# Kernel tuning notes

Measured on AMD Instinct MI355X. Metric: run time of the kernel, lower is better.

Reference implementation:

```python
import jax, jax.numpy as jnp
import numpy as np

N = 50000
E = 600000
IN_DIM = 128
D = 32          # out_dim per head
H = 4           # heads
M = 3           # num metapaths
HID = 128       # semantic attention hidden
NEG_SLOPE = 0.2


def setup_inputs() -> dict:
    key = jax.random.key(0)
    ks = jax.random.split(key, 12)
    x = jax.random.normal(ks[0], (N, IN_DIM), dtype=jnp.float32)
    mp_edge_index = jax.random.randint(ks[1], (M, 2, E), 0, N, dtype=jnp.int64)
    s = 1.0 / np.sqrt(IN_DIM)
    W = jax.random.normal(ks[2], (M, IN_DIM, H * D), dtype=jnp.float32) * s
    att_src = jax.random.normal(ks[3], (M, H, D), dtype=jnp.float32) * (1.0 / np.sqrt(D))
    att_dst = jax.random.normal(ks[4], (M, H, D), dtype=jnp.float32) * (1.0 / np.sqrt(D))
    bias = jnp.zeros((M, H * D), dtype=jnp.float32)
    ln_gamma = jnp.ones((H * D,), dtype=jnp.float32)
    ln_beta = jnp.zeros((H * D,), dtype=jnp.float32)
    sem_W1 = jax.random.normal(ks[5], (H * D, HID), dtype=jnp.float32) * (1.0 / np.sqrt(H * D))
    sem_b1 = jnp.zeros((HID,), dtype=jnp.float32)
    sem_W2 = jax.random.normal(ks[6], (HID, 1), dtype=jnp.float32) * (1.0 / np.sqrt(HID))
    return dict(x=x, mp_edge_index=mp_edge_index, W=W, att_src=att_src,
                att_dst=att_dst, bias=bias, ln_gamma=ln_gamma, ln_beta=ln_beta,
                sem_W1=sem_W1, sem_b1=sem_b1, sem_W2=sem_W2)


def _gat_conv(x, edge_index, W_m, a_src, a_dst, b_m):
    # PyG GATConv (add_self_loops=True, concat=True). x: [N, F_in]
    n = x.shape[0]
    h = (x @ W_m).reshape(n, H, D)                       # [N, H, D]
    loops = jnp.arange(n, dtype=edge_index.dtype)
    src = jnp.concatenate([edge_index[0], loops])        # [E+N]
    dst = jnp.concatenate([edge_index[1], loops])
    alpha_s = jnp.einsum('nhd,hd->nh', h, a_src)         # [N, H]
    alpha_d = jnp.einsum('nhd,hd->nh', h, a_dst)
    e = jax.nn.leaky_relu(alpha_s[src] + alpha_d[dst], NEG_SLOPE)  # [E+N, H]
    # segment softmax over edges grouped by destination node
    e_max = jax.ops.segment_max(e, dst, num_segments=n)
    e = jnp.exp(e - e_max[dst])
    denom = jax.ops.segment_sum(e, dst, num_segments=n)
    alpha = e / (denom[dst] + 1e-16)                     # [E+N, H]
    msg = h[src] * alpha[:, :, None]                     # [E+N, H, D]
    out = jax.ops.segment_sum(msg, dst, num_segments=n)  # [N, H, D]
    return out.reshape(n, H * D) + b_m


def _layer_norm(y, gamma, beta):
    mu = y.mean(-1, keepdims=True)
    var = y.var(-1, keepdims=True)
    return (y - mu) * jax.lax.rsqrt(var + 1e-5) * gamma + beta


def reference(x, mp_edge_index, W, att_src, att_dst, bias, ln_gamma, ln_beta,
              sem_W1, sem_b1, sem_W2):
    embs = []
    for i in range(M):
        emb = _gat_conv(x, mp_edge_index[i], W[i], att_src[i], att_dst[i], bias[i])
        emb = jax.nn.elu(_layer_norm(emb, ln_gamma, ln_beta))
        embs.append(emb)
    z = jnp.stack(embs, axis=1)                          # [N, M, H*D]
    # semantic attention
    w = (jnp.tanh(z @ sem_W1 + sem_b1) @ sem_W2).mean(0)  # [M, 1]
    beta = jax.nn.softmax(w, axis=0)                      # [M, 1]
    out_emb = (beta[None, :, :] * z).sum(1)               # [N, H*D]
    att_mp = beta.squeeze()                               # [M]
    return out_emb, att_mp
```

## Files before the change

### kernel.cpp

```cpp
#include <hip/hip_runtime.h>
#include <hip/hip_bf16.h>

#define N_NODES 50000
#define N_EDGES 600000
#define NMETA   3
#define NEG_SLOPE 0.2f
#define LTOT (NMETA * N_NODES)
#define SPAN_SHIFT 9
#define NBUCK 98
#define BCAP 8192

typedef unsigned short u16;
typedef short bf16x8 __attribute__((ext_vector_type(8)));
typedef float f32x4 __attribute__((ext_vector_type(4)));

__device__ __forceinline__ float bf2f(u16 v) {
    union { unsigned int u; float f; } x; x.u = ((unsigned int)v) << 16; return x.f;
}
__device__ __forceinline__ u16 f2bf(float f) {
    return __hip_bfloat16_raw(__float2bfloat16(f)).x;
}

__global__ __launch_bounds__(256) void k_prep_x(
    const float* __restrict__ x, u16* __restrict__ xb)
{
    int i = blockIdx.x * 256 + threadIdx.x;
    if (i >= N_NODES * 32) return;
    float4 v = ((const float4*)x)[i];
    ushort4 o;
    o.x = f2bf(v.x); o.y = f2bf(v.y); o.z = f2bf(v.z); o.w = f2bf(v.w);
    ((ushort4*)xb)[i] = o;
}

__global__ __launch_bounds__(256) void k_prep_w(
    const float* __restrict__ W, const float* __restrict__ W1,
    u16* __restrict__ WT, u16* __restrict__ W1T)
{
    int idx = blockIdx.x * 256 + threadIdx.x;
    if (idx < NMETA * 16384) {
        int m = idx >> 14, r = idx & 16383;
        int col = r >> 7, k = r & 127;
        WT[idx] = f2bf(W[(m << 14) + k * 128 + col]);
    } else {
        int r = idx - NMETA * 16384;
        int col = r >> 7, k = r & 127;
        W1T[r] = f2bf(W1[k * 128 + col]);
    }
}

__global__ __launch_bounds__(256) void k_gemm_h(
    const u16* __restrict__ xb,
    const u16* __restrict__ WT,
    const float* __restrict__ att_src,
    const float* __restrict__ att_dst,
    u16* __restrict__ h,
    float* __restrict__ alpha_s,
    float* __restrict__ alpha_d)
{
    const int m = blockIdx.y;
    const int wv = threadIdx.x >> 6, lane = threadIdx.x & 63;
    const int row0 = (blockIdx.x * 4 + wv) * 16;
    if (row0 >= N_NODES) return;
    const int lhi = lane >> 4, llo = lane & 15;
    const u16* xrow = xb + (size_t)(row0 + llo) * 128 + lhi * 8;
    bf16x8 a[4];
    #pragma unroll
    for (int ks = 0; ks < 4; ++ks) a[ks] = *(const bf16x8*)(xrow + ks * 32);
    const u16* wbase = WT + (size_t)m * 16384 + (size_t)llo * 128 + lhi * 8;
    u16* hm = h + ((size_t)m * N_NODES + row0) * 128;
    float sp[4][4], dp[4][4];
    #pragma unroll
    for (int i = 0; i < 4; ++i)
        #pragma unroll
        for (int r = 0; r < 4; ++r) { sp[i][r] = 0.f; dp[i][r] = 0.f; }
    #pragma unroll
    for (int cf = 0; cf < 8; ++cf) {
        f32x4 acc = {0.f, 0.f, 0.f, 0.f};
        const u16* wp = wbase + cf * 16 * 128;
        #pragma unroll
        for (int ks = 0; ks < 4; ++ks) {
            bf16x8 b = *(const bf16x8*)(wp + ks * 32);
            acc = __builtin_amdgcn_mfma_f32_16x16x32_bf16(a[ks], b, acc, 0, 0, 0);
        }
        const int col = cf * 16 + llo;
        const int hh = cf >> 1;
        const float as = att_src[m * 128 + col];
        const float ad = att_dst[m * 128 + col];
        #pragma unroll
        for (int r = 0; r < 4; ++r) {
            hm[(size_t)(lhi * 4 + r) * 128 + col] = f2bf(acc[r]);
            sp[hh][r] += acc[r] * as;
            dp[hh][r] += acc[r] * ad;
        }
    }
    #pragma unroll
    for (int o = 1; o <= 8; o <<= 1) {
        #pragma unroll
        for (int i = 0; i < 4; ++i)
            #pragma unroll
            for (int r = 0; r < 4; ++r) {
                sp[i][r] += __shfl_xor(sp[i][r], o);
                dp[i][r] += __shfl_xor(dp[i][r], o);
            }
    }
    if (llo == 0) {
        #pragma unroll
        for (int r = 0; r < 4; ++r) {
            int n = row0 + lhi * 4 + r;
            f32x4 vs = {sp[0][r], sp[1][r], sp[2][r], sp[3][r]};
            f32x4 vd = {dp[0][r], dp[1][r], dp[2][r], dp[3][r]};
            *(f32x4*)(alpha_s + ((size_t)m * N_NODES + n) * 4) = vs;
            *(f32x4*)(alpha_d + ((size_t)m * N_NODES + n) * 4) = vd;
        }
    }
}

__global__ __launch_bounds__(256) void k_csrA(
    const int* __restrict__ ei, int* __restrict__ gcnt,
    unsigned long long* __restrict__ pairs)
{
    const int m = blockIdx.y;
    __shared__ int cnt[NBUCK];
    __shared__ int gbase[NBUCK];
    const int t = threadIdx.x;
    if (t < NBUCK) cnt[t] = 0;
    __syncthreads();
    const int e0 = blockIdx.x * 4096;
    const int* srcp = ei + (size_t)m * 2 * N_EDGES;
    const int* dstp = srcp + N_EDGES;
    int sa[16], da[16], sl[16];
    #pragma unroll
    for (int j = 0; j < 16; ++j) {
        int e = e0 + j * 256 + t;
        if (e < N_EDGES) {
            int s = srcp[e], d = dstp[e];
            if ((unsigned)s >= N_NODES) s = 0;
            if ((unsigned)d >= N_NODES) d = 0;
            sa[j] = s; da[j] = d;
            sl[j] = atomicAdd(&cnt[d >> SPAN_SHIFT], 1);
        } else sl[j] = -1;
    }
    __syncthreads();
    if (t < NBUCK) gbase[t] = atomicAdd(&gcnt[m * NBUCK + t], cnt[t]);
    __syncthreads();
    #pragma unroll
    for (int j = 0; j < 16; ++j) {
        if (sl[j] < 0) continue;
        int b = da[j] >> SPAN_SHIFT;
        int pos = gbase[b] + sl[j];
        if (pos < BCAP)
            pairs[(size_t)(m * NBUCK + b) * BCAP + pos] =
                ((unsigned long long)(da[j] & 511) << 32) | (unsigned)(sa[j] * 128);
    }
}

__global__ __launch_bounds__(256) void k_csrB(
    const int* __restrict__ gcnt, const unsigned long long* __restrict__ pairs,
    int* __restrict__ row_start, int* __restrict__ row_end, int* __restrict__ eidx)
{
    const int m = blockIdx.y, b = blockIdx.x;
    const int t = threadIdx.x;
    __shared__ int cnt[512];
    __shared__ int off[512];
    __shared__ int wsum[4];
    int nb = gcnt[m * NBUCK + b]; if (nb > BCAP) nb = BCAP;
    const int base = (m * NBUCK + b) * BCAP;
    cnt[t] = 0; cnt[t + 256] = 0;
    __syncthreads();
    for (int e = t; e < nb; e += 256) {
        int dl = (int)(pairs[(size_t)base + e] >> 32);
        atomicAdd(&cnt[dl], 1);
    }
    __syncthreads();
    int v0 = cnt[2 * t], v1 = cnt[2 * t + 1];
    int s = v0 + v1;
    int lane = t & 63, wv = t >> 6;
    int incl = s;
    #pragma unroll
    for (int o = 1; o < 64; o <<= 1) {
        int u = __shfl_up(incl, o);
        if (lane >= o) incl += u;
    }
    if (lane == 63) wsum[wv] = incl;
    __syncthreads();
    int woff = 0;
    for (int i = 0; i < wv; ++i) woff += wsum[i];
    int ex = woff + incl - s;
    off[2 * t] = ex;
    off[2 * t + 1] = ex + v0;
    __syncthreads();
    const int node0 = b << SPAN_SHIFT;
    for (int i = t; i < 512; i += 256) {
        int n = node0 + i;
        if (n < N_NODES) {
            int st = base + off[i];
            row_start[m * N_NODES + n] = st;
            row_end[m * N_NODES + n]   = st + cnt[i];
        }
    }
    __syncthreads();
    for (int e = t; e < nb; e += 256) {
        unsigned long long p = pairs[(size_t)base + e];
        int dl = (int)(p >> 32);
        int pos = atomicAdd(&off[dl], 1);
        eidx[(size_t)base + pos] = (int)(unsigned)p;
    }
}

__global__ __launch_bounds__(256) void k_gather(
    const int* __restrict__ row_start, const int* __restrict__ row_end,
    const int* __restrict__ eidx,
    const float* __restrict__ alpha_s, const float* __restrict__ alpha_d,
    const u16* __restrict__ h,
    const float* __restrict__ bias, const float* __restrict__ gamma,
    const float* __restrict__ lbeta,
    u16* __restrict__ z)
{
    long long w = ((long long)blockIdx.x * blockDim.x + threadIdx.x) >> 6;
    if (w >= (long long)LTOT) return;
    int m = (int)(w / N_NODES), n = (int)(w % N_NODES);
    int lane = threadIdx.x & 63, hh = lane >> 4;
    const float* as_m = alpha_s + (size_t)m * N_NODES * 4;
    const float* ad_m = alpha_d + (size_t)m * N_NODES * 4;
    const u16*   h_m  = h + (size_t)m * N_NODES * 128;
    float ad = ad_m[n * 4 + hh];
    float pre = as_m[n * 4 + hh] + ad;
    pre = pre > 0.f ? pre : NEG_SLOPE * pre;
    float ev = __expf(pre);
    float esum = ev;
    ushort2 hv = *(const ushort2*)(h_m + n * 128 + lane * 2);
    float acc0 = ev * bf2f(hv.x), acc1 = ev * bf2f(hv.y);
    int p = row_start[m * N_NODES + n];
    const int end = row_end[m * N_NODES + n];
    for (; p + 3 < end; p += 4) {
        int o1 = eidx[p], o2 = eidx[p + 1], o3 = eidx[p + 2], o4 = eidx[p + 3];
        float p1 = as_m[(o1 >> 5) + hh] + ad;
        float p2 = as_m[(o2 >> 5) + hh] + ad;
        float p3 = as_m[(o3 >> 5) + hh] + ad;
        float p4 = as_m[(o4 >> 5) + hh] + ad;
        ushort2 h1 = *(const ushort2*)(h_m + o1 + lane * 2);
        ushort2 h2 = *(const ushort2*)(h_m + o2 + lane * 2);
        ushort2 h3 = *(const ushort2*)(h_m + o3 + lane * 2);
        ushort2 h4 = *(const ushort2*)(h_m + o4 + lane * 2);
        p1 = p1 > 0.f ? p1 : NEG_SLOPE * p1;
        p2 = p2 > 0.f ? p2 : NEG_SLOPE * p2;
        p3 = p3 > 0.f ? p3 : NEG_SLOPE * p3;
        p4 = p4 > 0.f ? p4 : NEG_SLOPE * p4;
        float e1 = __expf(p1), e2 = __expf(p2), e3 = __expf(p3), e4 = __expf(p4);
        esum += (e1 + e2) + (e3 + e4);
        acc0 += e1 * bf2f(h1.x) + e2 * bf2f(h2.x) + e3 * bf2f(h3.x) + e4 * bf2f(h4.x);
        acc1 += e1 * bf2f(h1.y) + e2 * bf2f(h2.y) + e3 * bf2f(h3.y) + e4 * bf2f(h4.y);
    }
    for (; p < end; ++p) {
        int o1 = eidx[p];
        float p1 = as_m[(o1 >> 5) + hh] + ad;
        ushort2 h1 = *(const ushort2*)(h_m + o1 + lane * 2);
        p1 = p1 > 0.f ? p1 : NEG_SLOPE * p1;
        float e1 = __expf(p1);
        esum += e1;
        acc0 += e1 * bf2f(h1.x);
        acc1 += e1 * bf2f(h1.y);
    }
    float rinv = 1.f / (esum + 1e-16f);
    float v0 = acc0 * rinv + bias[m * 128 + lane * 2];
    float v1 = acc1 * rinv + bias[m * 128 + lane * 2 + 1];
    float s1 = v0 + v1, s2 = v0 * v0 + v1 * v1;
    #pragma unroll
    for (int o = 32; o >= 1; o >>= 1) { s1 += __shfl_xor(s1, o); s2 += __shfl_xor(s2, o); }
    float mu = s1 * (1.f / 128.f);
    float var = s2 * (1.f / 128.f) - mu * mu;
    float rs = rsqrtf(var + 1e-5f);
    float o0 = (v0 - mu) * rs * gamma[lane * 2]     + lbeta[lane * 2];
    float o1 = (v1 - mu) * rs * gamma[lane * 2 + 1] + lbeta[lane * 2 + 1];
    o0 = o0 > 0.f ? o0 : (__expf(o0) - 1.f);
    o1 = o1 > 0.f ? o1 : (__expf(o1) - 1.f);
    ushort2 outv; outv.x = f2bf(o0); outv.y = f2bf(o1);
    *(ushort2*)(z + ((size_t)n * NMETA + m) * 128 + lane * 2) = outv;
}

__global__ __launch_bounds__(256) void k_sem(
    const u16* __restrict__ z,
    const u16* __restrict__ W1T,
    const float* __restrict__ b1,
    const float* __restrict__ W2,
    float* __restrict__ wpart)
{
    __shared__ float part[NMETA];
    const int t = threadIdx.x;
    if (t < NMETA) part[t] = 0.f;
    __syncthreads();
    const int wv = t >> 6, lane = t & 63;
    const int row0 = (blockIdx.x * 4 + wv) * 16;
    if (row0 < LTOT) {
        const int lhi = lane >> 4, llo = lane & 15;
        const u16* zrow = z + (size_t)(row0 + llo) * 128 + lhi * 8;
        bf16x8 a[4];
        #pragma unroll
        for (int ks = 0; ks < 4; ++ks) a[ks] = *(const bf16x8*)(zrow + ks * 32);
        const u16* wb = W1T + (size_t)llo * 128 + lhi * 8;
        float rowacc[4] = {0.f, 0.f, 0.f, 0.f};
        #pragma unroll
        for (int cf = 0; cf < 8; ++cf) {
            f32x4 acc = {0.f, 0.f, 0.f, 0.f};
            const u16* wp = wb + cf * 16 * 128;
            #pragma unroll
            for (int ks = 0; ks < 4; ++ks) {
                bf16x8 bb = *(const bf16x8*)(wp + ks * 32);
                acc = __builtin_amdgcn_mfma_f32_16x16x32_bf16(a[ks], bb, acc, 0, 0, 0);
            }
            int col = cf * 16 + llo;
            float b1v = b1[col], w2v = W2[col];
            #pragma unroll
            for (int r = 0; r < 4; ++r)
                rowacc[r] += tanhf(acc[r] + b1v) * w2v;
        }
        #pragma unroll
        for (int o = 1; o <= 8; o <<= 1) {
            #pragma unroll
            for (int r = 0; r < 4; ++r) rowacc[r] += __shfl_xor(rowacc[r], o);
        }
        if (llo == 0) {
            #pragma unroll
            for (int r = 0; r < 4; ++r)
                atomicAdd(&part[(row0 + lhi * 4 + r) % NMETA], rowacc[r]);
        }
    }
    __syncthreads();
    if (t < NMETA) atomicAdd(&wpart[t], part[t]);
}

__global__ void k_beta(const float* __restrict__ wpart, float* __restrict__ betab,
                       float* __restrict__ attout)
{
    if (threadIdx.x == 0 && blockIdx.x == 0) {
        float w0 = wpart[0] * (1.f / N_NODES);
        float w1 = wpart[1] * (1.f / N_NODES);
        float w2 = wpart[2] * (1.f / N_NODES);
        float mx = fmaxf(w0, fmaxf(w1, w2));
        float e0 = __expf(w0 - mx), e1 = __expf(w1 - mx), e2 = __expf(w2 - mx);
        float s = 1.f / (e0 + e1 + e2);
        float b0 = e0 * s, b1 = e1 * s, b2 = e2 * s;
        betab[0] = b0; betab[1] = b1; betab[2] = b2;
        attout[0] = b0; attout[1] = b1; attout[2] = b2;
    }
}

__global__ __launch_bounds__(256) void k_combine(
    const u16* __restrict__ z, const float* __restrict__ betab,
    float* __restrict__ out)
{
    int idx = blockIdx.x * blockDim.x + threadIdx.x;
    if (idx >= N_NODES * 64) return;
    int n = idx >> 6, c2 = (idx & 63) * 2;
    float b0 = betab[0], b1 = betab[1], b2 = betab[2];
    const u16* zp = z + (size_t)n * NMETA * 128 + c2;
    ushort2 a0 = *(const ushort2*)(zp);
    ushort2 a1 = *(const ushort2*)(zp + 128);
    ushort2 a2 = *(const ushort2*)(zp + 256);
    float2 ov;
    ov.x = b0 * bf2f(a0.x) + b1 * bf2f(a1.x) + b2 * bf2f(a2.x);
    ov.y = b0 * bf2f(a0.y) + b1 * bf2f(a1.y) + b2 * bf2f(a2.y);
    *(float2*)(out + (size_t)n * 128 + c2) = ov;
}

extern "C" void kernel_launch(void* const* d_in, const int* in_sizes, int n_in,
                              void* d_out, int out_size, void* d_ws, size_t ws_size,
                              hipStream_t stream) {
    const float* x       = (const float*)d_in[0];
    const int*   ei      = (const int*)d_in[1];
    const float* W       = (const float*)d_in[2];
    const float* att_src = (const float*)d_in[3];
    const float* att_dst = (const float*)d_in[4];
    const float* bias    = (const float*)d_in[5];
    const float* gamma   = (const float*)d_in[6];
    const float* lbeta   = (const float*)d_in[7];
    const float* W1      = (const float*)d_in[8];
    const float* b1      = (const float*)d_in[9];
    const float* W2      = (const float*)d_in[10];

    char* ws = (char*)d_ws;
    size_t off = 0;
    int* gcnt    = (int*)(ws + off);  off += sizeof(int) * 512;
    float* wpart = (float*)(ws + off);
    float* betab = wpart + 8;         off += 64;
    const size_t zero_bytes = off;
    off = (off + 255) & ~(size_t)255;
    int* row_start = (int*)(ws + off); off += sizeof(int) * 150016;
    int* row_end   = (int*)(ws + off); off += sizeof(int) * 150016;
    u16* h      = (u16*)(ws + off);    off += sizeof(u16) * (size_t)NMETA * N_NODES * 128;
    float* alpha_s = (float*)(ws + off); off += sizeof(float) * (size_t)LTOT * 4;
    float* alpha_d = (float*)(ws + off); off += sizeof(float) * (size_t)LTOT * 4;
    u16* z      = (u16*)(ws + off);    off += sizeof(u16) * (size_t)N_NODES * NMETA * 128;
    u16* WT     = (u16*)(ws + off);    off += sizeof(u16) * (size_t)NMETA * 128 * 128;
    u16* W1T    = (u16*)(ws + off);    off += sizeof(u16) * (size_t)128 * 128;
    int* eidx   = (int*)(ws + off);    off += sizeof(int) * (size_t)NMETA * NBUCK * BCAP;
    u16* xb = (u16*)(ws + off);
    unsigned long long* pairs = (unsigned long long*)(ws + off);
    off += sizeof(unsigned long long) * (size_t)NMETA * NBUCK * BCAP;
    if (ws_size < off) return;

    hipMemsetAsync(d_ws, 0, zero_bytes, stream);

    k_prep_x<<<dim3(N_NODES * 32 / 256), 256, 0, stream>>>(x, xb);
    k_prep_w<<<dim3(256), 256, 0, stream>>>(W, W1, WT, W1T);
    k_gemm_h<<<dim3((N_NODES / 16 + 3) / 4, NMETA), 256, 0, stream>>>(
        xb, WT, att_src, att_dst, h, alpha_s, alpha_d);
    k_csrA<<<dim3((N_EDGES + 4095) / 4096, NMETA), 256, 0, stream>>>(ei, gcnt, pairs);
    k_csrB<<<dim3(NBUCK, NMETA), 256, 0, stream>>>(gcnt, pairs, row_start, row_end, eidx);
    k_gather<<<dim3((LTOT + 3) / 4), 256, 0, stream>>>(row_start, row_end, eidx,
                                                       alpha_s, alpha_d, h,
                                                       bias, gamma, lbeta, z);
    k_sem<<<dim3((LTOT / 16 + 3) / 4), 256, 0, stream>>>(z, W1T, b1, W2, wpart);
    k_beta<<<1, 64, 0, stream>>>(wpart, betab, (float*)d_out + (size_t)N_NODES * 128);
    k_combine<<<dim3((N_NODES * 64 + 255) / 256), 256, 0, stream>>>(z, betab, (float*)d_out);
}
```

Baseline: 289.0 us.

## Fuse x conversion into GEMM, loop metapaths per block, lane-parallel edge softmax

The separate x-to-bf16 kernel is removed and each GEMM block converts its x rows itself. The block then loops over all three metapaths, reusing the A fragments so x is read once instead of three times. The attention logits are pre-scaled by log2(e) so the gather can use exp2f. The gather now assigns one edge-head pair to each lane for 16 edges at a time, then broadcasts weights and offsets by shuffle, instead of every lane computing every exponential redundantly. The cost is a fixed 16-iteration inner loop that issues dummy loads on padded slots, and the z buffer now shares memory with the dead pairs buffer.

```diff
diff --git a/kernel.cpp b/kernel.cpp
--- a/kernel.cpp
+++ b/kernel.cpp
@@ -4,11 +4,11 @@
 #define N_NODES 50000
 #define N_EDGES 600000
 #define NMETA   3
-#define NEG_SLOPE 0.2f
 #define LTOT (NMETA * N_NODES)
 #define SPAN_SHIFT 9
 #define NBUCK 98
 #define BCAP 8192
+#define LOG2E 1.4426950408889634f
 
 typedef unsigned short u16;
 typedef short bf16x8 __attribute__((ext_vector_type(8)));
@@ -19,17 +19,6 @@
 }
 __device__ __forceinline__ u16 f2bf(float f) {
     return __hip_bfloat16_raw(__float2bfloat16(f)).x;
-}
-
-__global__ __launch_bounds__(256) void k_prep_x(
-    const float* __restrict__ x, u16* __restrict__ xb)
-{
-    int i = blockIdx.x * 256 + threadIdx.x;
-    if (i >= N_NODES * 32) return;
-    float4 v = ((const float4*)x)[i];
-    ushort4 o;
-    o.x = f2bf(v.x); o.y = f2bf(v.y); o.z = f2bf(v.z); o.w = f2bf(v.w);
-    ((ushort4*)xb)[i] = o;
 }
 
 __global__ __launch_bounds__(256) void k_prep_w(
@@ -49,7 +38,7 @@
 }
 
 __global__ __launch_bounds__(256) void k_gemm_h(
-    const u16* __restrict__ xb,
+    const float* __restrict__ x,
     const u16* __restrict__ WT,
     const float* __restrict__ att_src,
     const float* __restrict__ att_dst,
@@ -57,60 +46,68 @@
     float* __restrict__ alpha_s,
     float* __restrict__ alpha_d)
 {
-    const int m = blockIdx.y;
     const int wv = threadIdx.x >> 6, lane = threadIdx.x & 63;
     const int row0 = (blockIdx.x * 4 + wv) * 16;
     if (row0 >= N_NODES) return;
     const int lhi = lane >> 4, llo = lane & 15;
-    const u16* xrow = xb + (size_t)(row0 + llo) * 128 + lhi * 8;
+    const float* xrow = x + (size_t)(row0 + llo) * 128 + lhi * 8;
     bf16x8 a[4];
     #pragma unroll
-    for (int ks = 0; ks < 4; ++ks) a[ks] = *(const bf16x8*)(xrow + ks * 32);
-    const u16* wbase = WT + (size_t)m * 16384 + (size_t)llo * 128 + lhi * 8;
-    u16* hm = h + ((size_t)m * N_NODES + row0) * 128;
-    float sp[4][4], dp[4][4];
-    #pragma unroll
-    for (int i = 0; i < 4; ++i)
-        #pragma unroll
-        for (int r = 0; r < 4; ++r) { sp[i][r] = 0.f; dp[i][r] = 0.f; }
-    #pragma unroll
-    for (int cf = 0; cf < 8; ++cf) {
-        f32x4 acc = {0.f, 0.f, 0.f, 0.f};
-        const u16* wp = wbase + cf * 16 * 128;
-        #pragma unroll
-        for (int ks = 0; ks < 4; ++ks) {
-            bf16x8 b = *(const bf16x8*)(wp + ks * 32);
-            acc = __builtin_amdgcn_mfma_f32_16x16x32_bf16(a[ks], b, acc, 0, 0, 0);
-        }
-        const int col = cf * 16 + llo;
-        const int hh = cf >> 1;
-        const float as = att_src[m * 128 + col];
-        const float ad = att_dst[m * 128 + col];
-        #pragma unroll
-        for (int r = 0; r < 4; ++r) {
-            hm[(size_t)(lhi * 4 + r) * 128 + col] = f2bf(acc[r]);
-            sp[hh][r] += acc[r] * as;
-            dp[hh][r] += acc[r] * ad;
-        }
-    }
-    #pragma unroll
-    for (int o = 1; o <= 8; o <<= 1) {
+    for (int ks = 0; ks < 4; ++ks) {
+        float4 f0 = *(const float4*)(xrow + ks * 32);
+        float4 f1 = *(const float4*)(xrow + ks * 32 + 4);
+        bf16x8 av;
+        av[0] = f2bf(f0.x); av[1] = f2bf(f0.y); av[2] = f2bf(f0.z); av[3] = f2bf(f0.w);
+        av[4] = f2bf(f1.x); av[5] = f2bf(f1.y); av[6] = f2bf(f1.z); av[7] = f2bf(f1.w);
+        a[ks] = av;
+    }
+    for (int m = 0; m < NMETA; ++m) {
+        const u16* wbase = WT + (size_t)m * 16384 + (size_t)llo * 128 + lhi * 8;
+        u16* hm = h + ((size_t)m * N_NODES + row0) * 128;
+        float sp[4][4], dp[4][4];
         #pragma unroll
         for (int i = 0; i < 4; ++i)
             #pragma unroll
+            for (int r = 0; r < 4; ++r) { sp[i][r] = 0.f; dp[i][r] = 0.f; }
+        #pragma unroll
+        for (int cf = 0; cf < 8; ++cf) {
+            f32x4 acc = {0.f, 0.f, 0.f, 0.f};
+            const u16* wp = wbase + cf * 16 * 128;
+            #pragma unroll
+            for (int ks = 0; ks < 4; ++ks) {
+                bf16x8 b = *(const bf16x8*)(wp + ks * 32);
+                acc = __builtin_amdgcn_mfma_f32_16x16x32_bf16(a[ks], b, acc, 0, 0, 0);
+            }
+            const int col = cf * 16 + llo;
+            const int hh = cf >> 1;
+            const float as = att_src[m * 128 + col];
+            const float adv = att_dst[m * 128 + col];
+            #pragma unroll
             for (int r = 0; r < 4; ++r) {
-                sp[i][r] += __shfl_xor(sp[i][r], o);
-                dp[i][r] += __shfl_xor(dp[i][r], o);
+                hm[(size_t)(lhi * 4 + r) * 128 + col] = f2bf(acc[r]);
+                sp[hh][r] += acc[r] * as;
+                dp[hh][r] += acc[r] * adv;
             }
-    }
-    if (llo == 0) {
-        #pragma unroll
-        for (int r = 0; r < 4; ++r) {
-            int n = row0 + lhi * 4 + r;
-            f32x4 vs = {sp[0][r], sp[1][r], sp[2][r], sp[3][r]};
-            f32x4 vd = {dp[0][r], dp[1][r], dp[2][r], dp[3][r]};
-            *(f32x4*)(alpha_s + ((size_t)m * N_NODES + n) * 4) = vs;
-            *(f32x4*)(alpha_d + ((size_t)m * N_NODES + n) * 4) = vd;
+        }
+        #pragma unroll
+        for (int o = 1; o <= 8; o <<= 1) {
+            #pragma unroll
+            for (int i = 0; i < 4; ++i)
+                #pragma unroll
+                for (int r = 0; r < 4; ++r) {
+                    sp[i][r] += __shfl_xor(sp[i][r], o);
+                    dp[i][r] += __shfl_xor(dp[i][r], o);
+                }
+        }
+        if (llo == 0) {
+            #pragma unroll
+            for (int r = 0; r < 4; ++r) {
+                int n = row0 + lhi * 4 + r;
+                f32x4 vs = {sp[0][r] * LOG2E, sp[1][r] * LOG2E, sp[2][r] * LOG2E, sp[3][r] * LOG2E};
+                f32x4 vd = {dp[0][r] * LOG2E, dp[1][r] * LOG2E, dp[2][r] * LOG2E, dp[3][r] * LOG2E};
+                *(f32x4*)(alpha_s + ((size_t)m * N_NODES + n) * 4) = vs;
+                *(f32x4*)(alpha_d + ((size_t)m * N_NODES + n) * 4) = vd;
+            }
         }
     }
 }
@@ -219,48 +216,46 @@
     long long w = ((long long)blockIdx.x * blockDim.x + threadIdx.x) >> 6;
     if (w >= (long long)LTOT) return;
     int m = (int)(w / N_NODES), n = (int)(w % N_NODES);
-    int lane = threadIdx.x & 63, hh = lane >> 4;
+    int lane = threadIdx.x & 63;
+    int hh = lane >> 4;
+    int hc = lane & 3;
     const float* as_m = alpha_s + (size_t)m * N_NODES * 4;
     const float* ad_m = alpha_d + (size_t)m * N_NODES * 4;
     const u16*   h_m  = h + (size_t)m * N_NODES * 128;
-    float ad = ad_m[n * 4 + hh];
-    float pre = as_m[n * 4 + hh] + ad;
-    pre = pre > 0.f ? pre : NEG_SLOPE * pre;
-    float ev = __expf(pre);
-    float esum = ev;
+    float pre_s = as_m[n * 4 + hh] + ad_m[n * 4 + hh];
+    pre_s = fmaxf(pre_s, 0.2f * pre_s);
+    float e_self = exp2f(pre_s);
     ushort2 hv = *(const ushort2*)(h_m + n * 128 + lane * 2);
-    float acc0 = ev * bf2f(hv.x), acc1 = ev * bf2f(hv.y);
-    int p = row_start[m * N_NODES + n];
-    const int end = row_end[m * N_NODES + n];
-    for (; p + 3 < end; p += 4) {
-        int o1 = eidx[p], o2 = eidx[p + 1], o3 = eidx[p + 2], o4 = eidx[p + 3];
-        float p1 = as_m[(o1 >> 5) + hh] + ad;
-        float p2 = as_m[(o2 >> 5) + hh] + ad;
-        float p3 = as_m[(o3 >> 5) + hh] + ad;
-        float p4 = as_m[(o4 >> 5) + hh] + ad;
-        ushort2 h1 = *(const ushort2*)(h_m + o1 + lane * 2);
-        ushort2 h2 = *(const ushort2*)(h_m + o2 + lane * 2);
-        ushort2 h3 = *(const ushort2*)(h_m + o3 + lane * 2);
-        ushort2 h4 = *(const ushort2*)(h_m + o4 + lane * 2);
-        p1 = p1 > 0.f ? p1 : NEG_SLOPE * p1;
-        p2 = p2 > 0.f ? p2 : NEG_SLOPE * p2;
-        p3 = p3 > 0.f ? p3 : NEG_SLOPE * p3;
-        p4 = p4 > 0.f ? p4 : NEG_SLOPE * p4;
-        float e1 = __expf(p1), e2 = __expf(p2), e3 = __expf(p3), e4 = __expf(p4);
-        esum += (e1 + e2) + (e3 + e4);
-        acc0 += e1 * bf2f(h1.x) + e2 * bf2f(h2.x) + e3 * bf2f(h3.x) + e4 * bf2f(h4.x);
-        acc1 += e1 * bf2f(h1.y) + e2 * bf2f(h2.y) + e3 * bf2f(h3.y) + e4 * bf2f(h4.y);
-    }
-    for (; p < end; ++p) {
-        int o1 = eidx[p];
-        float p1 = as_m[(o1 >> 5) + hh] + ad;
-        ushort2 h1 = *(const ushort2*)(h_m + o1 + lane * 2);
-        p1 = p1 > 0.f ? p1 : NEG_SLOPE * p1;
-        float e1 = __expf(p1);
-        esum += e1;
-        acc0 += e1 * bf2f(h1.x);
-        acc1 += e1 * bf2f(h1.y);
-    }
+    float acc0 = e_self * bf2f(hv.x), acc1 = e_self * bf2f(hv.y);
+    float ad_hc = ad_m[n * 4 + hc];
+    const int start = row_start[m * N_NODES + n];
+    const int end   = row_end[m * N_NODES + n];
+    float esum_l = 0.f;
+    for (int p = start; p < end; p += 16) {
+        int ep = p + (lane >> 2);
+        int off = 0;
+        float e = 0.f;
+        if (ep < end) {
+            off = eidx[ep];
+            float pre = as_m[(off >> 5) + hc] + ad_hc;
+            pre = fmaxf(pre, 0.2f * pre);
+            e = exp2f(pre);
+        }
+        esum_l += e;
+        #pragma unroll
+        for (int j = 0; j < 16; ++j) {
+            float eb = __shfl(e, j * 4 + hh);
+            int   ob = __shfl(off, j * 4);
+            ushort2 hj = *(const ushort2*)(h_m + ob + lane * 2);
+            acc0 += eb * bf2f(hj.x);
+            acc1 += eb * bf2f(hj.y);
+        }
+    }
+    esum_l += __shfl_xor(esum_l, 4);
+    esum_l += __shfl_xor(esum_l, 8);
+    esum_l += __shfl_xor(esum_l, 16);
+    esum_l += __shfl_xor(esum_l, 32);
+    float esum = __shfl(esum_l, hh) + e_self;
     float rinv = 1.f / (esum + 1e-16f);
     float v0 = acc0 * rinv + bias[m * 128 + lane * 2];
     float v1 = acc1 * rinv + bias[m * 128 + lane * 2 + 1];
@@ -390,21 +385,19 @@
     u16* h      = (u16*)(ws + off);    off += sizeof(u16) * (size_t)NMETA * N_NODES * 128;
     float* alpha_s = (float*)(ws + off); off += sizeof(float) * (size_t)LTOT * 4;
     float* alpha_d = (float*)(ws + off); off += sizeof(float) * (size_t)LTOT * 4;
-    u16* z      = (u16*)(ws + off);    off += sizeof(u16) * (size_t)N_NODES * NMETA * 128;
     u16* WT     = (u16*)(ws + off);    off += sizeof(u16) * (size_t)NMETA * 128 * 128;
     u16* W1T    = (u16*)(ws + off);    off += sizeof(u16) * (size_t)128 * 128;
     int* eidx   = (int*)(ws + off);    off += sizeof(int) * (size_t)NMETA * NBUCK * BCAP;
-    u16* xb = (u16*)(ws + off);
     unsigned long long* pairs = (unsigned long long*)(ws + off);
-    off += sizeof(unsigned long long) * (size_t)NMETA * NBUCK * BCAP;
+    u16* z = (u16*)(ws + off);
+    off += sizeof(u16) * (size_t)N_NODES * NMETA * 128;
     if (ws_size < off) return;
 
     hipMemsetAsync(d_ws, 0, zero_bytes, stream);
 
-    k_prep_x<<<dim3(N_NODES * 32 / 256), 256, 0, stream>>>(x, xb);
     k_prep_w<<<dim3(256), 256, 0, stream>>>(W, W1, WT, W1T);
-    k_gemm_h<<<dim3((N_NODES / 16 + 3) / 4, NMETA), 256, 0, stream>>>(
-        xb, WT, att_src, att_dst, h, alpha_s, alpha_d);
+    k_gemm_h<<<dim3((N_NODES / 16 + 3) / 4), 256, 0, stream>>>(
+        x, WT, att_src, att_dst, h, alpha_s, alpha_d);
     k_csrA<<<dim3((N_EDGES + 4095) / 4096, NMETA), 256, 0, stream>>>(ei, gcnt, pairs);
     k_csrB<<<dim3(NBUCK, NMETA), 256, 0, stream>>>(gcnt, pairs, row_start, row_end, eidx);
     k_gather<<<dim3((LTOT + 3) / 4), 256, 0, stream>>>(row_start, row_end, eidx,
```

New measurement: 297.3 us. 1.03x slower.

## Merge prep, CSR build and GEMM kernels into two launches, use exp2

Applied to the files above, without the earlier changes.

Cuts the launch sequence from five kernels to two. The weight transpose now runs alongside CSR bucketing, and the bf16 GEMM runs alongside CSR finalisation as separate block ranges of one grid. The x-to-bf16 conversion is folded into the GEMM's operand loads, which drops the xb buffer and its round trip through memory. Attention logits are pre-scaled by log2(e) so the gather can use exp2f and a fmax-based leaky ReLU, and z now aliases the pairs buffer to shrink the workspace. The risks are heterogeneous blocks within one grid, which can unbalance scheduling, and a reuse of pairs that is only safe if nothing reads it after build2.

```diff
diff --git a/kernel.cpp b/kernel.cpp
--- a/kernel.cpp
+++ b/kernel.cpp
@@ -4,11 +4,12 @@
 #define N_NODES 50000
 #define N_EDGES 600000
 #define NMETA   3
-#define NEG_SLOPE 0.2f
 #define LTOT (NMETA * N_NODES)
 #define SPAN_SHIFT 9
 #define NBUCK 98
 #define BCAP 8192
+#define NCHUNK 147
+#define LOG2E 1.4426950408889634f
 
 typedef unsigned short u16;
 typedef short bf16x8 __attribute__((ext_vector_type(8)));
@@ -21,111 +22,33 @@
     return __hip_bfloat16_raw(__float2bfloat16(f)).x;
 }
 
-__global__ __launch_bounds__(256) void k_prep_x(
-    const float* __restrict__ x, u16* __restrict__ xb)
-{
-    int i = blockIdx.x * 256 + threadIdx.x;
-    if (i >= N_NODES * 32) return;
-    float4 v = ((const float4*)x)[i];
-    ushort4 o;
-    o.x = f2bf(v.x); o.y = f2bf(v.y); o.z = f2bf(v.z); o.w = f2bf(v.w);
-    ((ushort4*)xb)[i] = o;
-}
-
-__global__ __launch_bounds__(256) void k_prep_w(
+__global__ __launch_bounds__(256) void k_build1(
+    const int* __restrict__ ei, int* __restrict__ gcnt,
+    unsigned long long* __restrict__ pairs,
     const float* __restrict__ W, const float* __restrict__ W1,
     u16* __restrict__ WT, u16* __restrict__ W1T)
 {
-    int idx = blockIdx.x * 256 + threadIdx.x;
-    if (idx < NMETA * 16384) {
-        int m = idx >> 14, r = idx & 16383;
-        int col = r >> 7, k = r & 127;
-        WT[idx] = f2bf(W[(m << 14) + k * 128 + col]);
-    } else {
-        int r = idx - NMETA * 16384;
-        int col = r >> 7, k = r & 127;
-        W1T[r] = f2bf(W1[k * 128 + col]);
-    }
-}
-
-__global__ __launch_bounds__(256) void k_gemm_h(
-    const u16* __restrict__ xb,
-    const u16* __restrict__ WT,
-    const float* __restrict__ att_src,
-    const float* __restrict__ att_dst,
-    u16* __restrict__ h,
-    float* __restrict__ alpha_s,
-    float* __restrict__ alpha_d)
-{
-    const int m = blockIdx.y;
-    const int wv = threadIdx.x >> 6, lane = threadIdx.x & 63;
-    const int row0 = (blockIdx.x * 4 + wv) * 16;
-    if (row0 >= N_NODES) return;
-    const int lhi = lane >> 4, llo = lane & 15;
-    const u16* xrow = xb + (size_t)(row0 + llo) * 128 + lhi * 8;
-    bf16x8 a[4];
-    #pragma unroll
-    for (int ks = 0; ks < 4; ++ks) a[ks] = *(const bf16x8*)(xrow + ks * 32);
-    const u16* wbase = WT + (size_t)m * 16384 + (size_t)llo * 128 + lhi * 8;
-    u16* hm = h + ((size_t)m * N_NODES + row0) * 128;
-    float sp[4][4], dp[4][4];
-    #pragma unroll
-    for (int i = 0; i < 4; ++i)
-        #pragma unroll
-        for (int r = 0; r < 4; ++r) { sp[i][r] = 0.f; dp[i][r] = 0.f; }
-    #pragma unroll
-    for (int cf = 0; cf < 8; ++cf) {
-        f32x4 acc = {0.f, 0.f, 0.f, 0.f};
-        const u16* wp = wbase + cf * 16 * 128;
-        #pragma unroll
-        for (int ks = 0; ks < 4; ++ks) {
-            bf16x8 b = *(const bf16x8*)(wp + ks * 32);
-            acc = __builtin_amdgcn_mfma_f32_16x16x32_bf16(a[ks], b, acc, 0, 0, 0);
-        }
-        const int col = cf * 16 + llo;
-        const int hh = cf >> 1;
-        const float as = att_src[m * 128 + col];
-        const float ad = att_dst[m * 128 + col];
-        #pragma unroll
-        for (int r = 0; r < 4; ++r) {
-            hm[(size_t)(lhi * 4 + r) * 128 + col] = f2bf(acc[r]);
-            sp[hh][r] += acc[r] * as;
-            dp[hh][r] += acc[r] * ad;
-        }
-    }
-    #pragma unroll
-    for (int o = 1; o <= 8; o <<= 1) {
-        #pragma unroll
-        for (int i = 0; i < 4; ++i)
-            #pragma unroll
-            for (int r = 0; r < 4; ++r) {
-                sp[i][r] += __shfl_xor(sp[i][r], o);
-                dp[i][r] += __shfl_xor(dp[i][r], o);
-            }
-    }
-    if (llo == 0) {
-        #pragma unroll
-        for (int r = 0; r < 4; ++r) {
-            int n = row0 + lhi * 4 + r;
-            f32x4 vs = {sp[0][r], sp[1][r], sp[2][r], sp[3][r]};
-            f32x4 vd = {dp[0][r], dp[1][r], dp[2][r], dp[3][r]};
-            *(f32x4*)(alpha_s + ((size_t)m * N_NODES + n) * 4) = vs;
-            *(f32x4*)(alpha_d + ((size_t)m * N_NODES + n) * 4) = vd;
-        }
-    }
-}
-
-__global__ __launch_bounds__(256) void k_csrA(
-    const int* __restrict__ ei, int* __restrict__ gcnt,
-    unsigned long long* __restrict__ pairs)
-{
-    const int m = blockIdx.y;
+    const int bid = blockIdx.x;
+    const int t = threadIdx.x;
+    if (bid >= NMETA * NCHUNK) {
+        int idx = (bid - NMETA * NCHUNK) * 256 + t;
+        if (idx < NMETA * 16384) {
+            int m = idx >> 14, r = idx & 16383;
+            int col = r >> 7, k = r & 127;
+            WT[idx] = f2bf(W[(m << 14) + k * 128 + col]);
+        } else {
+            int r = idx - NMETA * 16384;
+            int col = r >> 7, k = r & 127;
+            W1T[r] = f2bf(W1[k * 128 + col]);
+        }
+        return;
+    }
+    const int m = bid / NCHUNK;
+    const int e0 = (bid % NCHUNK) * 4096;
     __shared__ int cnt[NBUCK];
     __shared__ int gbase[NBUCK];
-    const int t = threadIdx.x;
     if (t < NBUCK) cnt[t] = 0;
     __syncthreads();
-    const int e0 = blockIdx.x * 4096;
     const int* srcp = ei + (size_t)m * 2 * N_EDGES;
     const int* dstp = srcp + N_EDGES;
     int sa[16], da[16], sl[16];
@@ -154,56 +77,127 @@
     }
 }
 
-__global__ __launch_bounds__(256) void k_csrB(
+__global__ __launch_bounds__(256) void k_build2(
     const int* __restrict__ gcnt, const unsigned long long* __restrict__ pairs,
-    int* __restrict__ row_start, int* __restrict__ row_end, int* __restrict__ eidx)
-{
-    const int m = blockIdx.y, b = blockIdx.x;
+    int* __restrict__ row_start, int* __restrict__ row_end, int* __restrict__ eidx,
+    const float* __restrict__ x, const u16* __restrict__ WT,
+    const float* __restrict__ att_src, const float* __restrict__ att_dst,
+    u16* __restrict__ h, float* __restrict__ alpha_s, float* __restrict__ alpha_d)
+{
+    const int bid = blockIdx.x;
     const int t = threadIdx.x;
-    __shared__ int cnt[512];
-    __shared__ int off[512];
-    __shared__ int wsum[4];
-    int nb = gcnt[m * NBUCK + b]; if (nb > BCAP) nb = BCAP;
-    const int base = (m * NBUCK + b) * BCAP;
-    cnt[t] = 0; cnt[t + 256] = 0;
-    __syncthreads();
-    for (int e = t; e < nb; e += 256) {
-        int dl = (int)(pairs[(size_t)base + e] >> 32);
-        atomicAdd(&cnt[dl], 1);
-    }
-    __syncthreads();
-    int v0 = cnt[2 * t], v1 = cnt[2 * t + 1];
-    int s = v0 + v1;
-    int lane = t & 63, wv = t >> 6;
-    int incl = s;
-    #pragma unroll
-    for (int o = 1; o < 64; o <<= 1) {
-        int u = __shfl_up(incl, o);
-        if (lane >= o) incl += u;
-    }
-    if (lane == 63) wsum[wv] = incl;
-    __syncthreads();
-    int woff = 0;
-    for (int i = 0; i < wv; ++i) woff += wsum[i];
-    int ex = woff + incl - s;
-    off[2 * t] = ex;
-    off[2 * t + 1] = ex + v0;
-    __syncthreads();
-    const int node0 = b << SPAN_SHIFT;
-    for (int i = t; i < 512; i += 256) {
-        int n = node0 + i;
-        if (n < N_NODES) {
-            int st = base + off[i];
-            row_start[m * N_NODES + n] = st;
-            row_end[m * N_NODES + n]   = st + cnt[i];
-        }
-    }
-    __syncthreads();
-    for (int e = t; e < nb; e += 256) {
-        unsigned long long p = pairs[(size_t)base + e];
-        int dl = (int)(p >> 32);
-        int pos = atomicAdd(&off[dl], 1);
-        eidx[(size_t)base + pos] = (int)(unsigned)p;
+    if (bid < NMETA * NBUCK) {
+        const int m = bid / NBUCK, b = bid % NBUCK;
+        __shared__ int cnt[512];
+        __shared__ int off[512];
+        __shared__ int wsum[4];
+        int nb = gcnt[m * NBUCK + b]; if (nb > BCAP) nb = BCAP;
+        const int base = (m * NBUCK + b) * BCAP;
+        cnt[t] = 0; cnt[t + 256] = 0;
+        __syncthreads();
+        for (int e = t; e < nb; e += 256) {
+            int dl = (int)(pairs[(size_t)base + e] >> 32);
+            atomicAdd(&cnt[dl], 1);
+        }
+        __syncthreads();
+        int v0 = cnt[2 * t], v1 = cnt[2 * t + 1];
+        int s = v0 + v1;
+        int lane = t & 63, wv = t >> 6;
+        int incl = s;
+        #pragma unroll
+        for (int o = 1; o < 64; o <<= 1) {
+            int u = __shfl_up(incl, o);
+            if (lane >= o) incl += u;
+        }
+        if (lane == 63) wsum[wv] = incl;
+        __syncthreads();
+        int woff = 0;
+        for (int i = 0; i < wv; ++i) woff += wsum[i];
+        int ex = woff + incl - s;
+        off[2 * t] = ex;
+        off[2 * t + 1] = ex + v0;
+        __syncthreads();
+        const int node0 = b << SPAN_SHIFT;
+        for (int i = t; i < 512; i += 256) {
+            int n = node0 + i;
+            if (n < N_NODES) {
+                int st = base + off[i];
+                row_start[m * N_NODES + n] = st;
+                row_end[m * N_NODES + n]   = st + cnt[i];
+            }
+        }
+        __syncthreads();
+        for (int e = t; e < nb; e += 256) {
+            unsigned long long p = pairs[(size_t)base + e];
+            int dl = (int)(p >> 32);
+            int pos = atomicAdd(&off[dl], 1);
+            eidx[(size_t)base + pos] = (int)(unsigned)p;
+        }
+        return;
+    }
+    const int g = bid - NMETA * NBUCK;
+    const int bx = g % 782, m = g / 782;
+    const int wv = t >> 6, lane = t & 63;
+    const int row0 = (bx * 4 + wv) * 16;
+    if (row0 >= N_NODES) return;
+    const int lhi = lane >> 4, llo = lane & 15;
+    const float* xrow = x + (size_t)(row0 + llo) * 128 + lhi * 8;
+    bf16x8 a[4];
+    #pragma unroll
+    for (int ks = 0; ks < 4; ++ks) {
+        float4 f0 = *(const float4*)(xrow + ks * 32);
+        float4 f1 = *(const float4*)(xrow + ks * 32 + 4);
+        bf16x8 av;
+        av[0] = f2bf(f0.x); av[1] = f2bf(f0.y); av[2] = f2bf(f0.z); av[3] = f2bf(f0.w);
+        av[4] = f2bf(f1.x); av[5] = f2bf(f1.y); av[6] = f2bf(f1.z); av[7] = f2bf(f1.w);
+        a[ks] = av;
+    }
+    const u16* wbase = WT + (size_t)m * 16384 + (size_t)llo * 128 + lhi * 8;
+    u16* hm = h + ((size_t)m * N_NODES + row0) * 128;
+    float sp[4][4], dp[4][4];
+    #pragma unroll
+    for (int i = 0; i < 4; ++i)
+        #pragma unroll
+        for (int r = 0; r < 4; ++r) { sp[i][r] = 0.f; dp[i][r] = 0.f; }
+    #pragma unroll
+    for (int cf = 0; cf < 8; ++cf) {
+        f32x4 acc = {0.f, 0.f, 0.f, 0.f};
+        const u16* wp = wbase + cf * 16 * 128;
+        #pragma unroll
+        for (int ks = 0; ks < 4; ++ks) {
+            bf16x8 b = *(const bf16x8*)(wp + ks * 32);
+            acc = __builtin_amdgcn_mfma_f32_16x16x32_bf16(a[ks], b, acc, 0, 0, 0);
+        }
+        const int col = cf * 16 + llo;
+        const int hh = cf >> 1;
+        const float as = att_src[m * 128 + col];
+        const float adv = att_dst[m * 128 + col];
+        #pragma unroll
+        for (int r = 0; r < 4; ++r) {
+            hm[(size_t)(lhi * 4 + r) * 128 + col] = f2bf(acc[r]);
+            sp[hh][r] += acc[r] * as;
+            dp[hh][r] += acc[r] * adv;
+        }
+    }
+    #pragma unroll
+    for (int o = 1; o <= 8; o <<= 1) {
+        #pragma unroll
+        for (int i = 0; i < 4; ++i)
+            #pragma unroll
+            for (int r = 0; r < 4; ++r) {
+                sp[i][r] += __shfl_xor(sp[i][r], o);
+                dp[i][r] += __shfl_xor(dp[i][r], o);
+            }
+    }
+    if (llo == 0) {
+        #pragma unroll
+        for (int r = 0; r < 4; ++r) {
+            int n = row0 + lhi * 4 + r;
+            f32x4 vs = {sp[0][r] * LOG2E, sp[1][r] * LOG2E, sp[2][r] * LOG2E, sp[3][r] * LOG2E};
+            f32x4 vd = {dp[0][r] * LOG2E, dp[1][r] * LOG2E, dp[2][r] * LOG2E, dp[3][r] * LOG2E};
+            *(f32x4*)(alpha_s + ((size_t)m * N_NODES + n) * 4) = vs;
+            *(f32x4*)(alpha_d + ((size_t)m * N_NODES + n) * 4) = vd;
+        }
     }
 }
 
@@ -225,8 +219,8 @@
     const u16*   h_m  = h + (size_t)m * N_NODES * 128;
     float ad = ad_m[n * 4 + hh];
     float pre = as_m[n * 4 + hh] + ad;
-    pre = pre > 0.f ? pre : NEG_SLOPE * pre;
-    float ev = __expf(pre);
+    pre = fmaxf(pre, 0.2f * pre);
+    float ev = exp2f(pre);
     float esum = ev;
     ushort2 hv = *(const ushort2*)(h_m + n * 128 + lane * 2);
     float acc0 = ev * bf2f(hv.x), acc1 = ev * bf2f(hv.y);
@@ -242,11 +236,11 @@
         ushort2 h2 = *(const ushort2*)(h_m + o2 + lane * 2);
         ushort2 h3 = *(const ushort2*)(h_m + o3 + lane * 2);
         ushort2 h4 = *(const ushort2*)(h_m + o4 + lane * 2);
-        p1 = p1 > 0.f ? p1 : NEG_SLOPE * p1;
-        p2 = p2 > 0.f ? p2 : NEG_SLOPE * p2;
-        p3 = p3 > 0.f ? p3 : NEG_SLOPE * p3;
-        p4 = p4 > 0.f ? p4 : NEG_SLOPE * p4;
-        float e1 = __expf(p1), e2 = __expf(p2), e3 = __expf(p3), e4 = __expf(p4);
+        p1 = fmaxf(p1, 0.2f * p1);
+        p2 = fmaxf(p2, 0.2f * p2);
+        p3 = fmaxf(p3, 0.2f * p3);
+        p4 = fmaxf(p4, 0.2f * p4);
+        float e1 = exp2f(p1), e2 = exp2f(p2), e3 = exp2f(p3), e4 = exp2f(p4);
         esum += (e1 + e2) + (e3 + e4);
         acc0 += e1 * bf2f(h1.x) + e2 * bf2f(h2.x) + e3 * bf2f(h3.x) + e4 * bf2f(h4.x);
         acc1 += e1 * bf2f(h1.y) + e2 * bf2f(h2.y) + e3 * bf2f(h3.y) + e4 * bf2f(h4.y);
@@ -255,8 +249,8 @@
         int o1 = eidx[p];
         float p1 = as_m[(o1 >> 5) + hh] + ad;
         ushort2 h1 = *(const ushort2*)(h_m + o1 + lane * 2);
-        p1 = p1 > 0.f ? p1 : NEG_SLOPE * p1;
-        float e1 = __expf(p1);
+        p1 = fmaxf(p1, 0.2f * p1);
+        float e1 = exp2f(p1);
         esum += e1;
         acc0 += e1 * bf2f(h1.x);
         acc1 += e1 * bf2f(h1.y);
@@ -390,23 +384,20 @@
     u16* h      = (u16*)(ws + off);    off += sizeof(u16) * (size_t)NMETA * N_NODES * 128;
     float* alpha_s = (float*)(ws + off); off += sizeof(float) * (size_t)LTOT * 4;
     float* alpha_d = (float*)(ws + off); off += sizeof(float) * (size_t)LTOT * 4;
-    u16* z      = (u16*)(ws + off);    off += sizeof(u16) * (size_t)N_NODES * NMETA * 128;
     u16* WT     = (u16*)(ws + off);    off += sizeof(u16) * (size_t)NMETA * 128 * 128;
     u16* W1T    = (u16*)(ws + off);    off += sizeof(u16) * (size_t)128 * 128;
     int* eidx   = (int*)(ws + off);    off += sizeof(int) * (size_t)NMETA * NBUCK * BCAP;
-    u16* xb = (u16*)(ws + off);
     unsigned long long* pairs = (unsigned long long*)(ws + off);
-    off += sizeof(unsigned long long) * (size_t)NMETA * NBUCK * BCAP;
+    u16* z = (u16*)(ws + off);
+    off += sizeof(u16) * (size_t)N_NODES * NMETA * 128;
     if (ws_size < off) return;
 
     hipMemsetAsync(d_ws, 0, zero_bytes, stream);
 
-    k_prep_x<<<dim3(N_NODES * 32 / 256), 256, 0, stream>>>(x, xb);
-    k_prep_w<<<dim3(256), 256, 0, stream>>>(W, W1, WT, W1T);
-    k_gemm_h<<<dim3((N_NODES / 16 + 3) / 4, NMETA), 256, 0, stream>>>(
-        xb, WT, att_src, att_dst, h, alpha_s, alpha_d);
-    k_csrA<<<dim3((N_EDGES + 4095) / 4096, NMETA), 256, 0, stream>>>(ei, gcnt, pairs);
-    k_csrB<<<dim3(NBUCK, NMETA), 256, 0, stream>>>(gcnt, pairs, row_start, row_end, eidx);
+    k_build1<<<dim3(NMETA * NCHUNK + 256), 256, 0, stream>>>(ei, gcnt, pairs, W, W1, WT, W1T);
+    k_build2<<<dim3(NMETA * NBUCK + 782 * NMETA), 256, 0, stream>>>(
+        gcnt, pairs, row_start, row_end, eidx,
+        x, WT, att_src, att_dst, h, alpha_s, alpha_d);
     k_gather<<<dim3((LTOT + 3) / 4), 256, 0, stream>>>(row_start, row_end, eidx,
                                                        alpha_s, alpha_d, h,
                                                        bias, gamma, lbeta, z);
```

After: 274.2 us. 5.1% less time.
